# Kernel optimization log

Measured on AMD Instinct MI355X. Metric: run time of the kernel, lower is better.

## Reference

```python
import jax, jax.numpy as jnp
import numpy as np

# C2fBoT config (matches init_kwargs)
B, C1, C2, N, F, HEADS, E = 8, 512, 512, 2, 32, 4, 0.5
C = int(C2 * E)          # hidden channels = 256
HD = C // HEADS          # head_dim = 64
BN_EPS = 1e-3            # ultralytics Conv uses BatchNorm2d(eps=0.001)


def conv2d(x, w, pad):
    # x: [B,Cin,H,W], w: [Cout,Cin,kh,kw]
    return jax.lax.conv_general_dilated(
        x, w, (1, 1), [(pad, pad), (pad, pad)],
        dimension_numbers=("NCHW", "OIHW", "NCHW"))


def bn_eval(x, p):
    # p: [4,C] rows = gamma, beta, running_mean, running_var (inference BN)
    g, b, m, v = p
    s = (g / jnp.sqrt(v + BN_EPS))[:, None, None]
    return (x - m[:, None, None]) * s + b[:, None, None]


def cbs(x, w, p, pad):
    # YOLO Conv block: Conv2d -> BN -> SiLU
    return jax.nn.silu(bn_eval(conv2d(x, w, pad), p))


def bot_attention(x, qkv_w, rw, rh):
    # x: [B,C,H,W]; 1x1-conv QKV + learned relative position bias
    b, c, h, w = x.shape
    hw = h * w
    qkv = conv2d(x, qkv_w, 0).reshape(b, 3, HEADS, HD, hw)
    q, k, v = qkv[:, 0], qkv[:, 1], qkv[:, 2]           # [B,heads,hd,HW]
    r = (rw + rh).reshape(1, HEADS, HD, hw)              # rel-pos content
    # q^T@k*scale + q^T@r*scale == q^T@(k+r)*scale (r broadcasts over batch)
    logits = jnp.einsum('bhdi,bhdj->bhij', q, k + r) * (HD ** -0.5)
    a = jax.nn.softmax(logits, axis=-1)                  # [B,heads,HW,HW]
    out = jnp.einsum('bhij,bhdj->bhdi', a, v)            # [B,heads,hd,HW]
    return out.reshape(b, c, h, w)


def setup_inputs() -> dict:
    key = jax.random.key(0)
    ks = iter(jax.random.split(key, 32))
    def nrm(shape, s=0.05):
        return jax.random.normal(next(ks), shape, jnp.float32) * s
    def bnp(cc):
        return jnp.stack([
            1.0 + 0.1 * jax.random.normal(next(ks), (cc,), jnp.float32),  # gamma
            0.1 * jax.random.normal(next(ks), (cc,), jnp.float32),        # beta
            0.1 * jax.random.normal(next(ks), (cc,), jnp.float32),        # mean
            0.5 + jax.random.uniform(next(ks), (cc,), jnp.float32),       # var
        ])
    return {
        "x": jax.random.normal(next(ks), (B, C1, F, F), jnp.float32),
        "cv1_w": nrm((2 * C, C1, 1, 1)),
        "cv1_bn": bnp(2 * C),
        "cv2_w": nrm((C2, (2 + N) * C, 1, 1)),
        "cv2_bn": bnp(C2),
        "m_cv1_w": nrm((N, C, C, 3, 3)),
        "m_cv1_bn": jnp.stack([bnp(C) for _ in range(N)]),
        "m_qkv_w": nrm((N, 3 * C, C, 1, 1)),
        "m_rw": jax.random.normal(next(ks), (N, 1, HEADS, HD, 1, F), jnp.float32),
        "m_rh": jax.random.normal(next(ks), (N, 1, HEADS, HD, F, 1), jnp.float32),
        "m_cv2_w": nrm((N, C, C, 1, 1)),
        "m_cv2_bn": jnp.stack([bnp(C) for _ in range(N)]),
    }


def reference(x, cv1_w, cv1_bn, cv2_w, cv2_bn,
              m_cv1_w, m_cv1_bn, m_qkv_w, m_rw, m_rh, m_cv2_w, m_cv2_bn):
    t = cbs(x, cv1_w, cv1_bn, 0)                 # [B,2C,H,W]
    ys = [t[:, :C], t[:, C:]]                    # chunk(2, dim=1)
    for i in range(N):                           # fixed small layer loop
        yi = ys[-1]
        z = cbs(yi, m_cv1_w[i], m_cv1_bn[i], 1)  # 3x3 Conv-BN-SiLU
        z = bot_attention(z, m_qkv_w[i], m_rw[i], m_rh[i])
        z = jax.nn.silu(bn_eval(conv2d(z, m_cv2_w[i], 0), m_cv2_bn[i]))
        ys.append(yi + z)                        # shortcut (c1 == c2)
    return cbs(jnp.concatenate(ys, axis=1), cv2_w, cv2_bn, 0)
```

## Files before the change

### kernel.cpp

```cpp
#include <hip/hip_runtime.h>
#include <hip/hip_bf16.h>

typedef unsigned short ushort_t;
typedef __bf16 bf16x8 __attribute__((ext_vector_type(8)));
typedef float f32x4 __attribute__((ext_vector_type(4)));
typedef unsigned short us8 __attribute__((ext_vector_type(8)));
typedef unsigned int u32;

#define AS1 __attribute__((address_space(1)))
#define AS3 __attribute__((address_space(3)))

#if __has_builtin(__builtin_amdgcn_exp2f)
#define EXP2F __builtin_amdgcn_exp2f
#else
#define EXP2F exp2f
#endif

__device__ __forceinline__ void gld16(const void* g, void* l){
  __builtin_amdgcn_global_load_lds((AS1 void*)(void*)g, (AS3 void*)l, 16, 0, 0);
}
__device__ __forceinline__ f32x4 mfma16(bf16x8 a, bf16x8 b, f32x4 c){
  return __builtin_amdgcn_mfma_f32_16x16x32_bf16(a, b, c, 0, 0, 0);
}
__device__ __forceinline__ unsigned short f2bfu(float f){
  union { float f; unsigned int i; } c; c.f = f;
  unsigned int x = c.i;
  return (unsigned short)((x + 0x7fffu + ((x >> 16) & 1u)) >> 16);
}
__device__ __forceinline__ float bfu2f(unsigned short u){
  union { unsigned int i; float f; } c; c.i = ((unsigned int)u) << 16; return c.f;
}
__device__ __forceinline__ float dsilu(float x){ return x / (1.f + __expf(-x)); }
__device__ __forceinline__ u32 pack_trunc(float a, float b){
  union { float f; u32 u; } ca, cb; ca.f = a; cb.f = b;
#if __has_builtin(__builtin_amdgcn_perm)
  return __builtin_amdgcn_perm(cb.u, ca.u, 0x07060302u);
#else
  return (cb.u & 0xFFFF0000u) | (ca.u >> 16);
#endif
}

__global__ __launch_bounds__(256)
void prep_k(const float* __restrict__ x, ushort_t* __restrict__ xc,
            const float* __restrict__ s0, const float* __restrict__ s1,
            const float* __restrict__ s2, const float* __restrict__ s3,
            ushort_t* __restrict__ d0, ushort_t* __restrict__ d1,
            ushort_t* __restrict__ d2, ushort_t* __restrict__ d3,
            const float* __restrict__ w3, ushort_t* __restrict__ o3,
            ushort_t* __restrict__ zb)
{
  __shared__ float tl[64*68];
  const int bx = blockIdx.x, t = threadIdx.x;
  if (bx < 1024){
    const int b = bx >> 7, ci0 = (bx & 7)*64, px0 = ((bx >> 3) & 15)*64;
    {
      const int ci_l = t>>2, pc = (t&3)*16;
      const float* src = x + (size_t)b*524288 + (size_t)(ci0+ci_l)*1024 + px0 + pc;
      float* d = &tl[ci_l*68 + pc];
      *(float4*)(d)    = *(const float4*)(src);
      *(float4*)(d+4)  = *(const float4*)(src+4);
      *(float4*)(d+8)  = *(const float4*)(src+8);
      *(float4*)(d+12) = *(const float4*)(src+12);
    }
    __syncthreads();
    {
      const int px_l = t>>2, cc = (t&3)*16;
      us8 o0, o1;
#pragma unroll
      for (int i = 0; i < 8; i++) o0[i] = f2bfu(tl[(cc+i)*68 + px_l]);
#pragma unroll
      for (int i = 0; i < 8; i++) o1[i] = f2bfu(tl[(cc+8+i)*68 + px_l]);
      ushort_t* dst = xc + (size_t)b*524288 + (size_t)(px0+px_l)*512 + ci0 + cc;
      *(us8*)dst = o0; *(us8*)(dst+8) = o1;
    }
  } else if (bx < 2048){
    const int bb = bx - 1024;
    const int seg = bb >> 8, blk = bb & 255;
    const float* s = (seg==0?s0:seg==1?s1:seg==2?s2:s3);
    ushort_t* d    = (seg==0?d0:seg==1?d1:seg==2?d2:d3);
    const int n4   = (seg==0?262144:seg==1?524288:seg==2?393216:131072) >> 2;
    for (int i = blk*256 + t; i < n4; i += 256*256){
      const float4 v = *(const float4*)(s + (size_t)i*4);
      ushort4 p; p.x=f2bfu(v.x); p.y=f2bfu(v.y); p.z=f2bfu(v.z); p.w=f2bfu(v.w);
      *(ushort4*)(d + (size_t)i*4) = p;
    }
  } else {
    const int blk = bx - 2048;
    if (blk == 0 && t < 64) zb[t] = 0;
    const float* src = w3 + (size_t)blk*2304;
    ushort_t* dst = o3 + (size_t)blk*2304;
    for (int idx = t; idx < 2304; idx += 256){
      const int ci = idx/9, tap = idx - ci*9;
      dst[tap*256 + ci] = f2bfu(src[idx]);
    }
  }
}

template<int BMODE, int EPI, int NT>
__global__ __launch_bounds__(256, 4)
void gemm_k(const ushort_t* __restrict__ A, const int M, const int K, const int kplen,
            const ushort_t* __restrict__ B0, const ushort_t* __restrict__ B1,
            const ushort_t* __restrict__ B2, const ushort_t* __restrict__ B3,
            const int Rb, const long Bbs,
            const float* __restrict__ bnp,
            const float* __restrict__ rw, const float* __restrict__ rh,
            const ushort_t* __restrict__ res, const long res_bs, const int res_rs,
            ushort_t* __restrict__ vtout, const ushort_t* __restrict__ zb,
            void* __restrict__ outp, const long out_bs, const int out_rs)
{
  constexpr int NW = NT/4;
  constexpr int NF = NW/16;
  constexpr int CH = 8 + NT/8;
  constexpr int CPW = CH/4;
  const int m0 = blockIdx.x*64, n0 = blockIdx.y*NT;
  const int bz = blockIdx.z, b = bz & 7, part = bz >> 3;
  const int tid = threadIdx.x, lane = tid & 63, w = tid >> 6;
  const int q = lane >> 4, l15 = lane & 15;
  const int crow8 = lane >> 3, kq8 = lane & 7;
  const int gq8 = kq8 ^ crow8;
  const int r7 = l15 & 7;
  __shared__ __align__(16) ushort_t A_s[64*64];
  __shared__ __align__(16) ushort_t B_s[NT*64];

  f32x4 acc[4][NF];
#pragma unroll
  for (int mi = 0; mi < 4; mi++)
#pragma unroll
    for (int ni = 0; ni < NF; ni++) acc[mi][ni] = (f32x4){0.f,0.f,0.f,0.f};

  const int kbeg = part*kplen, kend_ = kbeg + kplen;
  for (int k0 = kbeg; k0 < kend_; k0 += 64){
    const int kk = k0 + gq8*8;
#pragma unroll
    for (int p = 0; p < CPW; p++){
      const int c = w*CPW + p;
      if (c < 8){
        const int row = c*8 + crow8;
        gld16(A + (size_t)(m0 + row)*K + kk, A_s + c*512);
      } else {
        const int cb = c - 8;
        const int row = cb*8 + crow8;
        const ushort_t* gb;
        if (BMODE == 0){
          gb = B0 + (size_t)b*Bbs + (size_t)(n0 + row)*Rb + kk;
        } else if (BMODE == 1){
          const int seg = kk >> 8;
          const ushort_t* sb = (seg==0?B0:seg==1?B1:seg==2?B2:B3);
          const int sstr = (seg < 2) ? 512 : 256;
          const long sbs = (seg < 2) ? 524288L : 262144L;
          gb = sb + (size_t)b*sbs + (size_t)(n0 + row)*sstr + (kk & 255);
        } else {
          const int tap = k0 >> 8;
          const int ci = (k0 & 255) + gq8*8;
          const int oy = tap/3 - 1, ox = tap - (tap/3)*3 - 1;
          const int px = n0 + row;
          const int yy = (px >> 5) + oy, xx = (px & 31) + ox;
          const bool vld = ((unsigned)yy < 32u) && ((unsigned)xx < 32u);
          gb = vld ? (B0 + (size_t)b*Bbs + (size_t)(yy*32 + xx)*Rb + ci) : zb;
        }
        gld16(gb, B_s + cb*512);
      }
    }
    __syncthreads();
#pragma unroll
    for (int ks = 0; ks < 2; ks++){
      const int slot = (ks*4 + q) ^ r7;
      bf16x8 af[4], bfr[NF];
#pragma unroll
      for (int mi = 0; mi < 4; mi++)
        af[mi] = __builtin_bit_cast(bf16x8, *(const us8*)&A_s[(mi*16 + l15)*64 + slot*8]);
#pragma unroll
      for (int ni = 0; ni < NF; ni++)
        bfr[ni] = __builtin_bit_cast(bf16x8, *(const us8*)&B_s[(w*NW + ni*16 + l15)*64 + slot*8]);
#pragma unroll
      for (int mi = 0; mi < 4; mi++)
#pragma unroll
        for (int ni = 0; ni < NF; ni++)
          acc[mi][ni] = mfma16(af[mi], bfr[ni], acc[mi][ni]);
    }
    __syncthreads();
  }

  const int n_w = n0 + w*NW;
#pragma unroll
  for (int mi = 0; mi < 4; mi++){
    const int mb = m0 + mi*16 + q*4;
    float sc[4], off[4];
    if (EPI != 1 && EPI != 4){
      const float4 g  = *(const float4*)(bnp + mb);
      const float4 be = *(const float4*)(bnp + M + mb);
      const float4 mu = *(const float4*)(bnp + 2*M + mb);
      const float4 va = *(const float4*)(bnp + 3*M + mb);
      sc[0] = g.x/sqrtf(va.x+1e-3f); off[0] = be.x - mu.x*sc[0];
      sc[1] = g.y/sqrtf(va.y+1e-3f); off[1] = be.y - mu.y*sc[1];
      sc[2] = g.z/sqrtf(va.z+1e-3f); off[2] = be.z - mu.z*sc[2];
      sc[3] = g.w/sqrtf(va.w+1e-3f); off[3] = be.w - mu.w*sc[3];
    }
    const int region = mb >> 8;
#pragma unroll
    for (int ni = 0; ni < NF; ni++){
      const int n_g = n_w + ni*16 + l15;
      f32x4 v = acc[mi][ni];
      if (EPI == 4){
        *(float4*)((float*)outp + ((size_t)(part*8 + b)*1024 + n_g)*256 + mb) =
            (float4){v[0], v[1], v[2], v[3]};
        continue;
      }
      float o[4];
#pragma unroll
      for (int r = 0; r < 4; r++){
        float xv = v[r];
        if (EPI == 1){
          if (region == 0) xv *= 0.18033688011112042f;
          else if (region == 1){
            const int c64 = mb + r - 256;
            xv += rw[c64*32 + (n_g & 31)] + rh[c64*32 + (n_g >> 5)];
          }
        } else {
          xv = dsilu(xv*sc[r] + off[r]);
          if (EPI == 2)
            xv += bfu2f(res[(size_t)b*res_bs + (size_t)n_g*res_rs + mb + r]);
        }
        o[r] = xv;
      }
      if (EPI == 3){
        float* of = (float*)outp + (size_t)b*out_bs;
#pragma unroll
        for (int r = 0; r < 4; r++) of[(size_t)(mb + r)*1024 + n_g] = o[r];
      } else if (EPI == 1 && region == 2){
#pragma unroll
        for (int r = 0; r < 4; r++)
          vtout[(size_t)b*262144 + (size_t)(mb + r - 512)*1024 + n_g] = f2bfu(o[r]);
      } else {
        ushort4 pk; pk.x=f2bfu(o[0]); pk.y=f2bfu(o[1]); pk.z=f2bfu(o[2]); pk.w=f2bfu(o[3]);
        *(ushort4*)((ushort_t*)outp + (size_t)b*out_bs + (size_t)n_g*out_rs + mb) = pk;
      }
    }
  }
}

__global__ __launch_bounds__(256)
void reduce3_k(const float* __restrict__ pbuf, const float* __restrict__ bnp,
               ushort_t* __restrict__ out)
{
  const int idx = blockIdx.x*256 + threadIdx.x;
  const int co = (idx & 63)*4;
  const size_t e = (size_t)idx*4;
  float4 a = *(const float4*)(pbuf + e);
  const float4 c = *(const float4*)(pbuf + 2097152 + e);
  a.x += c.x; a.y += c.y; a.z += c.z; a.w += c.w;
  const float4 g  = *(const float4*)(bnp + co);
  const float4 be = *(const float4*)(bnp + 256 + co);
  const float4 mu = *(const float4*)(bnp + 512 + co);
  const float4 va = *(const float4*)(bnp + 768 + co);
  float s0 = g.x/sqrtf(va.x+1e-3f), s1 = g.y/sqrtf(va.y+1e-3f);
  float s2 = g.z/sqrtf(va.z+1e-3f), s3 = g.w/sqrtf(va.w+1e-3f);
  ushort4 pk;
  pk.x = f2bfu(dsilu((a.x - mu.x)*s0 + be.x));
  pk.y = f2bfu(dsilu((a.y - mu.y)*s1 + be.y));
  pk.z = f2bfu(dsilu((a.z - mu.z)*s2 + be.z));
  pk.w = f2bfu(dsilu((a.w - mu.w)*s3 + be.w));
  *(ushort4*)(out + e) = pk;
}

__global__ __launch_bounds__(256)
void attn_k(const ushort_t* __restrict__ qk, const ushort_t* __restrict__ vt,
            ushort_t* __restrict__ out)
{
  const int it = blockIdx.x, h = blockIdx.y, b = blockIdx.z;
  const int tid = threadIdx.x, lane = tid & 63, w = tid >> 6;
  const int q = lane >> 4, l15 = lane & 15;
  const int i0 = it*64;
  __shared__ __align__(16) ushort_t K_s[2][8192];
  __shared__ __align__(16) ushort_t V_s[2][8192];
  __shared__ __align__(16) ushort_t P_s[8192];

  const ushort_t* qkb = qk + (size_t)b*524288;
  const ushort_t* vtb = vt + (size_t)b*262144 + (size_t)h*65536;

  const int k_row8 = lane >> 3;
  const int k_gq   = (lane & 7) ^ k_row8;
  const int v_row4 = lane >> 4;
  const int v_s16  = lane & 15;
  const int rs7    = l15 & 7;

  bf16x8 qf[2];
  {
    const ushort_t* qr = qkb + (size_t)(i0 + w*16 + l15)*512 + h*64 + q*8;
    qf[0] = __builtin_bit_cast(bf16x8, *(const us8*)qr);
    qf[1] = __builtin_bit_cast(bf16x8, *(const us8*)(qr + 32));
  }
  f32x4 oacc[4];
#pragma unroll
  for (int nd = 0; nd < 4; nd++) oacc[nd] = (f32x4){0.f,0.f,0.f,0.f};
  float m_s = -3e38f, l_s = 0.f;

#define STAGE(JT, BUF) {                                                        \
    const int j0s = (JT)*128;                                                   \
    _Pragma("unroll")                                                           \
    for (int p = 0; p < 4; p++){                                                \
      const int c = w*4 + p;                                                    \
      const int krow = c*8 + k_row8;                                            \
      gld16(qkb + (size_t)(j0s + krow)*512 + 256 + h*64 + k_gq*8, &K_s[BUF][c*512]); \
      const int vrow = c*4 + v_row4;                                            \
      const int vg = v_s16 ^ (vrow & 15);                                       \
      gld16(vtb + (size_t)vrow*1024 + j0s + vg*8, &V_s[BUF][c*512]);            \
    }                                                                           \
  }

  STAGE(0, 0);
  int cur = 0;
  for (int jt = 0; jt < 8; jt++){
    __syncthreads();
    if (jt < 7){ STAGE(jt+1, cur^1); }
    f32x4 sacc[8];
#pragma unroll
    for (int ni = 0; ni < 8; ni++) sacc[ni] = (f32x4){0.f,0.f,0.f,0.f};
#pragma unroll
    for (int ks = 0; ks < 2; ks++){
      const int slot = (ks*4 + q) ^ rs7;
#pragma unroll
      for (int ni = 0; ni < 8; ni++){
        const bf16x8 kf = __builtin_bit_cast(bf16x8,
            *(const us8*)&K_s[cur][(ni*16 + l15)*64 + slot*8]);
        sacc[ni] = mfma16(kf, qf[ks], sacc[ni]);
      }
    }
    float mx = sacc[0][0];
#pragma unroll
    for (int ni = 0; ni < 8; ni++)
#pragma unroll
      for (int r = 0; r < 4; r++) mx = fmaxf(mx, sacc[ni][r]);
    mx = fmaxf(mx, __shfl_xor(mx, 16));
    mx = fmaxf(mx, __shfl_xor(mx, 32));
    const float mnew = fmaxf(m_s, mx);
    const float alpha = EXP2F(m_s - mnew);
    m_s = mnew;
    float p[8][4];
    float ps = 0.f;
#pragma unroll
    for (int ni = 0; ni < 8; ni++)
#pragma unroll
      for (int r = 0; r < 4; r++){ p[ni][r] = EXP2F(sacc[ni][r] - mnew); ps += p[ni][r]; }
    ps += __shfl_xor(ps, 16);
    ps += __shfl_xor(ps, 32);
    l_s = l_s*alpha + ps;
#pragma unroll
    for (int r = 0; r < 4; r++){
      const float a_r = __shfl(alpha, q*4 + r);
#pragma unroll
      for (int nd = 0; nd < 4; nd++) oacc[nd][r] *= a_r;
    }
    {
      const int prow = w*16 + l15;
#pragma unroll
      for (int ni = 0; ni < 8; ni++){
        uint2 pk;
        pk.x = pack_trunc(p[ni][0], p[ni][1]);
        pk.y = pack_trunc(p[ni][2], p[ni][3]);
        const int phys = (ni*2 + (q>>1)) ^ l15;
        *(uint2*)&P_s[prow*128 + phys*8 + (q&1)*4] = pk;
      }
    }
#pragma unroll
    for (int ks = 0; ks < 4; ks++){
      const int slotp = (ks*4 + q) ^ l15;
      const bf16x8 pa = __builtin_bit_cast(bf16x8,
          *(const us8*)&P_s[(w*16 + l15)*128 + slotp*8]);
#pragma unroll
      for (int nd = 0; nd < 4; nd++){
        const bf16x8 vb = __builtin_bit_cast(bf16x8,
            *(const us8*)&V_s[cur][(nd*16 + l15)*128 + slotp*8]);
        oacc[nd] = mfma16(pa, vb, oacc[nd]);
      }
    }
    cur ^= 1;
  }
#undef STAGE
  ushort_t* ob = out + (size_t)b*262144;
#pragma unroll
  for (int r = 0; r < 4; r++){
    const float rinv = 1.f / __shfl(l_s, q*4 + r);
    const size_t rowo = (size_t)(i0 + w*16 + q*4 + r)*256 + h*64 + l15;
#pragma unroll
    for (int nd = 0; nd < 4; nd++)
      ob[rowo + nd*16] = f2bfu(oacc[nd][r]*rinv);
  }
}

extern "C" void kernel_launch(void* const* d_in, const int* in_sizes, int n_in,
                              void* d_out, int out_size, void* d_ws, size_t ws_size,
                              hipStream_t stream)
{
  const float* x       = (const float*)d_in[0];
  const float* cv1_w   = (const float*)d_in[1];
  const float* cv1_bn  = (const float*)d_in[2];
  const float* cv2_w   = (const float*)d_in[3];
  const float* cv2_bn  = (const float*)d_in[4];
  const float* mcv1_w  = (const float*)d_in[5];
  const float* mcv1_bn = (const float*)d_in[6];
  const float* mqkv_w  = (const float*)d_in[7];
  const float* mrw     = (const float*)d_in[8];
  const float* mrh     = (const float*)d_in[9];
  const float* mcv2_w  = (const float*)d_in[10];
  const float* mcv2_bn = (const float*)d_in[11];

  ushort_t* uw = (ushort_t*)d_ws;
  ushort_t* x_cl    = uw;
  ushort_t* t_cl    = x_cl    + 4194304;
  ushort_t* wb_cv1  = t_cl    + 4194304;
  ushort_t* wb_cv2  = wb_cv1  + 262144;
  ushort_t* wb_qkv  = wb_cv2  + 524288;
  ushort_t* wb_mcv2 = wb_qkv  + 393216;
  ushort_t* wb_mcv1 = wb_mcv2 + 131072;
  ushort_t* z1_cl   = wb_mcv1 + 1179648;
  ushort_t* qk_cl   = z1_cl   + 2097152;
  ushort_t* vt_b    = qk_cl   + 4194304;
  ushort_t* att_cl  = vt_b    + 2097152;
  ushort_t* y2_cl   = att_cl  + 2097152;
  ushort_t* y3_cl   = y2_cl   + 2097152;
  float*    part_f  = (float*)(y3_cl + 2097152);
  ushort_t* zbuf    = (ushort_t*)(part_f + 4194304);

  const dim3 blk(256);

  prep_k<<<dim3(2560), blk, 0, stream>>>(x, x_cl,
      cv1_w, cv2_w, mqkv_w, mcv2_w, wb_cv1, wb_cv2, wb_qkv, wb_mcv2,
      mcv1_w, wb_mcv1, zbuf);

  gemm_k<0,0,128><<<dim3(8,8,8), blk, 0, stream>>>(
      wb_cv1, 512, 512, 512, x_cl, nullptr, nullptr, nullptr, 512, 524288L,
      cv1_bn, nullptr, nullptr, nullptr, 0, 0, nullptr, nullptr, t_cl, 524288L, 512);

  const ushort_t* yi = t_cl + 256;  long yi_bs = 524288; int yi_rs = 512;
  ushort_t* youts[2] = { y2_cl, y3_cl };
  for (int i = 0; i < 2; i++){
    gemm_k<2,4,128><<<dim3(4,8,16), blk, 0, stream>>>(
        wb_mcv1 + (size_t)i*589824, 256, 2304, 1152, yi, nullptr, nullptr, nullptr,
        yi_rs, yi_bs,
        nullptr, nullptr, nullptr, nullptr, 0, 0, nullptr, zbuf, part_f, 0, 0);
    reduce3_k<<<dim3(2048), blk, 0, stream>>>(part_f, mcv1_bn + i*1024, z1_cl);
    gemm_k<0,1,128><<<dim3(12,8,8), blk, 0, stream>>>(
        wb_qkv + (size_t)i*196608, 768, 256, 256, z1_cl, nullptr, nullptr, nullptr, 256, 262144L,
        nullptr, mrw + i*8192, mrh + i*8192, nullptr, 0, 0, vt_b, nullptr, qk_cl, 524288L, 512);
    attn_k<<<dim3(16,4,8), blk, 0, stream>>>(qk_cl, vt_b, att_cl);
    gemm_k<0,2,64><<<dim3(4,16,8), blk, 0, stream>>>(
        wb_mcv2 + (size_t)i*65536, 256, 256, 256, att_cl, nullptr, nullptr, nullptr, 256, 262144L,
        mcv2_bn + i*1024, nullptr, nullptr, yi, yi_bs, yi_rs, nullptr, nullptr,
        youts[i], 262144L, 256);
    yi = youts[i]; yi_bs = 262144; yi_rs = 256;
  }

  gemm_k<1,3,128><<<dim3(8,8,8), blk, 0, stream>>>(
      wb_cv2, 512, 1024, 1024, t_cl, t_cl + 256, y2_cl, y3_cl, 0, 0,
      cv2_bn, nullptr, nullptr, nullptr, 0, 0, nullptr, nullptr, (float*)d_out, 524288L, 0);
}
```

Baseline: 295.3 us.

## Double-buffer GEMM k-loop and compute softmax row sums via MFMA

The GEMM kernel now stages the next K-slice into a second LDS buffer while the current one is multiplied, replacing two barriers per iteration with one so global loads overlap MFMA work. The attention kernel drops the per-tile shuffle-reduced row sum and instead accumulates the normalizer with an extra MFMA against a ones vector, using the truncated bf16 P values. This doubles GEMM LDS use, which may lower occupancy, and makes the normalizer match the bf16-rounded probabilities actually used in P·V.

```diff
diff --git a/kernel.cpp b/kernel.cpp
--- a/kernel.cpp
+++ b/kernel.cpp
@@ -119,8 +119,8 @@
   const int crow8 = lane >> 3, kq8 = lane & 7;
   const int gq8 = kq8 ^ crow8;
   const int r7 = l15 & 7;
-  __shared__ __align__(16) ushort_t A_s[64*64];
-  __shared__ __align__(16) ushort_t B_s[NT*64];
+  __shared__ __align__(16) ushort_t A_s[2][4096];
+  __shared__ __align__(16) ushort_t B_s[2][NT*64];
 
   f32x4 acc[4][NF];
 #pragma unroll
@@ -128,15 +128,14 @@
 #pragma unroll
     for (int ni = 0; ni < NF; ni++) acc[mi][ni] = (f32x4){0.f,0.f,0.f,0.f};
 
-  const int kbeg = part*kplen, kend_ = kbeg + kplen;
-  for (int k0 = kbeg; k0 < kend_; k0 += 64){
+  auto stage = [&](int k0, int buf){
     const int kk = k0 + gq8*8;
 #pragma unroll
     for (int p = 0; p < CPW; p++){
       const int c = w*CPW + p;
       if (c < 8){
         const int row = c*8 + crow8;
-        gld16(A + (size_t)(m0 + row)*K + kk, A_s + c*512);
+        gld16(A + (size_t)(m0 + row)*K + kk, &A_s[buf][c*512]);
       } else {
         const int cb = c - 8;
         const int row = cb*8 + crow8;
@@ -158,27 +157,34 @@
           const bool vld = ((unsigned)yy < 32u) && ((unsigned)xx < 32u);
           gb = vld ? (B0 + (size_t)b*Bbs + (size_t)(yy*32 + xx)*Rb + ci) : zb;
         }
-        gld16(gb, B_s + cb*512);
-      }
-    }
+        gld16(gb, &B_s[buf][cb*512]);
+      }
+    }
+  };
+
+  const int kbeg = part*kplen, kend_ = kbeg + kplen;
+  stage(kbeg, 0);
+  int cur = 0;
+  for (int k0 = kbeg; k0 < kend_; k0 += 64){
     __syncthreads();
+    if (k0 + 64 < kend_) stage(k0 + 64, cur ^ 1);
 #pragma unroll
     for (int ks = 0; ks < 2; ks++){
       const int slot = (ks*4 + q) ^ r7;
       bf16x8 af[4], bfr[NF];
 #pragma unroll
       for (int mi = 0; mi < 4; mi++)
-        af[mi] = __builtin_bit_cast(bf16x8, *(const us8*)&A_s[(mi*16 + l15)*64 + slot*8]);
+        af[mi] = __builtin_bit_cast(bf16x8, *(const us8*)&A_s[cur][(mi*16 + l15)*64 + slot*8]);
 #pragma unroll
       for (int ni = 0; ni < NF; ni++)
-        bfr[ni] = __builtin_bit_cast(bf16x8, *(const us8*)&B_s[(w*NW + ni*16 + l15)*64 + slot*8]);
+        bfr[ni] = __builtin_bit_cast(bf16x8, *(const us8*)&B_s[cur][(w*NW + ni*16 + l15)*64 + slot*8]);
 #pragma unroll
       for (int mi = 0; mi < 4; mi++)
 #pragma unroll
         for (int ni = 0; ni < NF; ni++)
           acc[mi][ni] = mfma16(af[mi], bfr[ni], acc[mi][ni]);
     }
-    __syncthreads();
+    cur ^= 1;
   }
 
   const int n_w = n0 + w*NW;
@@ -290,10 +296,14 @@
     qf[0] = __builtin_bit_cast(bf16x8, *(const us8*)qr);
     qf[1] = __builtin_bit_cast(bf16x8, *(const us8*)(qr + 32));
   }
+  const us8 ones_u = { 0x3F80,0x3F80,0x3F80,0x3F80,0x3F80,0x3F80,0x3F80,0x3F80 };
+  const bf16x8 onesf = __builtin_bit_cast(bf16x8, ones_u);
+
   f32x4 oacc[4];
 #pragma unroll
   for (int nd = 0; nd < 4; nd++) oacc[nd] = (f32x4){0.f,0.f,0.f,0.f};
-  float m_s = -3e38f, l_s = 0.f;
+  f32x4 lacc = (f32x4){0.f,0.f,0.f,0.f};
+  float m_s = -3e38f;
 
 #define STAGE(JT, BUF) {                                                        \
     const int j0s = (JT)*128;                                                   \
@@ -337,19 +347,16 @@
     const float alpha = EXP2F(m_s - mnew);
     m_s = mnew;
     float p[8][4];
-    float ps = 0.f;
 #pragma unroll
     for (int ni = 0; ni < 8; ni++)
 #pragma unroll
-      for (int r = 0; r < 4; r++){ p[ni][r] = EXP2F(sacc[ni][r] - mnew); ps += p[ni][r]; }
-    ps += __shfl_xor(ps, 16);
-    ps += __shfl_xor(ps, 32);
-    l_s = l_s*alpha + ps;
+      for (int r = 0; r < 4; r++) p[ni][r] = EXP2F(sacc[ni][r] - mnew);
 #pragma unroll
     for (int r = 0; r < 4; r++){
       const float a_r = __shfl(alpha, q*4 + r);
 #pragma unroll
       for (int nd = 0; nd < 4; nd++) oacc[nd][r] *= a_r;
+      lacc[r] *= a_r;
     }
     {
       const int prow = w*16 + l15;
@@ -367,6 +374,7 @@
       const int slotp = (ks*4 + q) ^ l15;
       const bf16x8 pa = __builtin_bit_cast(bf16x8,
           *(const us8*)&P_s[(w*16 + l15)*128 + slotp*8]);
+      lacc = mfma16(pa, onesf, lacc);
 #pragma unroll
       for (int nd = 0; nd < 4; nd++){
         const bf16x8 vb = __builtin_bit_cast(bf16x8,
@@ -380,7 +388,7 @@
   ushort_t* ob = out + (size_t)b*262144;
 #pragma unroll
   for (int r = 0; r < 4; r++){
-    const float rinv = 1.f / __shfl(l_s, q*4 + r);
+    const float rinv = 1.f / lacc[r];
     const size_t rowo = (size_t)(i0 + w*16 + q*4 + r)*256 + h*64 + l15;
 #pragma unroll
     for (int nd = 0; nd < 4; nd++)
```

Result: faster. 287.6 us (-2.6%).
